# Kernel optimization log

Hardware: AMD Instinct MI355X
Metric: run time of the kernel (lower is better)

The kernel has to match this reference:

```python
import jax, jax.numpy as jnp
import numpy as np

DIM = 1024
N_HEADS = 16
HEAD_DIM = DIM // N_HEADS


def setup_inputs() -> dict:
    key = jax.random.key(0)
    ks = jax.random.split(key, 5)
    B, L = 2, 2048
    q = jax.random.normal(ks[0], (B, L, DIM), dtype=jnp.float32)
    # nn.Linear weights: shape [out_features, in_features], applied as x @ W.T
    scale = 1.0 / np.sqrt(DIM)
    Wq = jax.random.normal(ks[1], (DIM, DIM), dtype=jnp.float32) * scale
    Wk = jax.random.normal(ks[2], (DIM, DIM), dtype=jnp.float32) * scale
    Wv = jax.random.normal(ks[3], (DIM, DIM), dtype=jnp.float32) * scale
    Wo = jax.random.normal(ks[4], (DIM, DIM), dtype=jnp.float32) * scale
    return {"q": q, "Wq": Wq, "Wk": Wk, "Wv": Wv, "Wo": Wo}


def reference(q, Wq, Wk, Wv, Wo):
    B, L, _ = q.shape
    kv = q  # self-attention (kv=None path)
    # projections: x @ W.T, then split heads: b l (h d) -> b h l d
    def split_heads(x):
        return x.reshape(B, L, N_HEADS, HEAD_DIM).transpose(0, 2, 1, 3)
    qh = split_heads(q @ Wq.T)
    kh = split_heads(kv @ Wk.T)
    vh = split_heads(kv @ Wv.T)
    # scaled dot-product attention; scale = sqrt(head_dim)
    scores = jnp.einsum('bhid,bhjd->bhij', qh, kh) / jnp.sqrt(
        jnp.asarray(HEAD_DIM, dtype=qh.dtype))
    attn = jax.nn.softmax(scores, axis=-1)
    out = jnp.einsum('bhij,bhjd->bhid', attn, vh)
    # b h l d -> b l (h d)
    out = out.transpose(0, 2, 1, 3).reshape(B, L, DIM)
    return out @ Wo.T
```

## Files before the change

kernel.cpp:

```cpp
#include <hip/hip_runtime.h>


#define DIMN 1024
#define NH 16
#define HD 64
#define BB 2
#define LL 2048

typedef float f32x4 __attribute__((ext_vector_type(4)));
typedef short s16x8 __attribute__((ext_vector_type(8)));

#define QSCALE 0.18033688011112042f

static __device__ __forceinline__ unsigned short f2bf(float f) {
  unsigned u = __float_as_uint(f);
  u += 0x7fffu + ((u >> 16) & 1u);
  return (unsigned short)(u >> 16);
}
static __device__ __forceinline__ unsigned packbf2(float lo, float hi) {
  return (unsigned)f2bf(lo) | ((unsigned)f2bf(hi) << 16);
}
static __device__ __forceinline__ float xexp2(float x) {
#if __has_builtin(__builtin_amdgcn_exp2f)
  return __builtin_amdgcn_exp2f(x);
#else
  return exp2f(x);
#endif
}
static __device__ __forceinline__ s16x8 cvt8(float4 a, float4 b) {
  s16x8 r;
  r[0] = (short)f2bf(a.x); r[1] = (short)f2bf(a.y);
  r[2] = (short)f2bf(a.z); r[3] = (short)f2bf(a.w);
  r[4] = (short)f2bf(b.x); r[5] = (short)f2bf(b.y);
  r[6] = (short)f2bf(b.z); r[7] = (short)f2bf(b.w);
  return r;
}
static __device__ __forceinline__ void gld16(const unsigned short* g,
                                             unsigned short* l) {
#if __has_builtin(__builtin_amdgcn_global_load_lds)
  __builtin_amdgcn_global_load_lds(
      (const __attribute__((address_space(1))) void*)g,
      (__attribute__((address_space(3))) void*)l, 16, 0, 0);
#else
  ((uint4*)l)[threadIdx.x & 63] = ((const uint4*)g)[0];
#endif
}

static __device__ __forceinline__ int vpos(int s128) {
  return (s128 & 0x60) | ((s128 & 0x0C) << 1) | ((s128 & 0x10) >> 2) | (s128 & 3);
}

__global__ __launch_bounds__(256) void cvt_all(
    const float* __restrict__ X, const float* __restrict__ Wq,
    const float* __restrict__ Wk, const float* __restrict__ Wv,
    const float* __restrict__ Wo, unsigned short* __restrict__ out) {
  const int blk = blockIdx.x;
  const float* src;
  unsigned short* dst;
  size_t off;
  if (blk < 2048) {
    src = X; dst = out; off = (size_t)blk * 2048;
  } else {
    int s = (blk - 2048) >> 9;
    src = (s == 0) ? Wq : (s == 1) ? Wk : (s == 2) ? Wv : Wo;
    dst = out + ((size_t)1 << 22) + (size_t)s * (1u << 20);
    off = (size_t)((blk - 2048) & 511) * 2048;
  }
  size_t i = off + (size_t)threadIdx.x * 8;
  float4 v0 = *(const float4*)(src + i);
  float4 v1 = *(const float4*)(src + i + 4);
  uint4 o;
  o.x = packbf2(v0.x, v0.y); o.y = packbf2(v0.z, v0.w);
  o.z = packbf2(v1.x, v1.y); o.w = packbf2(v1.z, v1.w);
  *(uint4*)(dst + i) = o;
}

__global__ __launch_bounds__(256) void gemm_qkv(
    const unsigned short* __restrict__ Xb, const unsigned short* __restrict__ Wb,
    unsigned short* __restrict__ Qb, unsigned short* __restrict__ Kb,
    unsigned short* __restrict__ VT) {
  __shared__ __align__(16) unsigned short Al[2][128 * 64];
  __shared__ __align__(16) unsigned short Bl[2][128 * 64];
  const int lin = blockIdx.x;
  const int xcd = lin & 7, sblk = lin >> 3;
  const int m0 = ((xcd & 3) * 8 + (sblk & 7)) * 128;
  const int n0g = ((xcd >> 2) * 12 + (sblk >> 3)) * 128;
  const int sel = n0g >> 10;
  const int tid = threadIdx.x;
  const int w = tid >> 6, lane = tid & 63;
  const int c = lane & 15, quad = lane >> 4;
  const int wm = (w & 1) * 64, wn = (w >> 1) * 64;

  f32x4 zero = {0.f, 0.f, 0.f, 0.f};
  f32x4 acc[4][4];
#pragma unroll
  for (int i = 0; i < 4; ++i)
#pragma unroll
    for (int j = 0; j < 4; ++j) acc[i][j] = zero;

  const int l8 = lane >> 3, p8 = lane & 7;
  const unsigned short* gA = Xb + (size_t)(m0 + w * 8 + l8) * DIMN + ((p8 ^ l8) * 8);
  const unsigned short* gB = Wb + (size_t)(n0g + w * 8 + l8) * DIMN + ((p8 ^ l8) * 8);
  const int c7 = c & 7;

#define STAGEQ(buf, k0)                                                       \
  do {                                                                        \
    unsigned short* lA_ = &Al[buf][(w * 8) * 64];                             \
    unsigned short* lB_ = &Bl[buf][(w * 8) * 64];                             \
    _Pragma("unroll")                                                         \
    for (int r = 0; r < 4; ++r) {                                             \
      gld16(gA + (k0) + (size_t)(r * 32) * DIMN, lA_ + r * 32 * 64);          \
      gld16(gB + (k0) + (size_t)(r * 32) * DIMN, lB_ + r * 32 * 64);          \
    }                                                                         \
  } while (0)

  STAGEQ(0, 0);
  __syncthreads();

  for (int t = 0; t < 16; ++t) {
    if (t < 15) STAGEQ((t + 1) & 1, (t + 1) * 64);
    const unsigned short* At = &Al[t & 1][0];
    const unsigned short* Bt = &Bl[t & 1][0];
#pragma unroll
    for (int f = 0; f < 2; ++f) {
      const int rd = ((f * 4 + quad) ^ c7) * 8;
      s16x8 a[4], b[4];
#pragma unroll
      for (int i = 0; i < 4; ++i)
        a[i] = *(const s16x8*)&At[(wm + i * 16 + c) * 64 + rd];
#pragma unroll
      for (int j = 0; j < 4; ++j)
        b[j] = *(const s16x8*)&Bt[(wn + j * 16 + c) * 64 + rd];
      if (sel != 2) {
#pragma unroll
        for (int i = 0; i < 4; ++i)
#pragma unroll
          for (int j = 0; j < 4; ++j)
            acc[i][j] = __builtin_amdgcn_mfma_f32_16x16x32_bf16(b[j], a[i], acc[i][j], 0, 0, 0);
      } else {
#pragma unroll
        for (int i = 0; i < 4; ++i)
#pragma unroll
          for (int j = 0; j < 4; ++j)
            acc[i][j] = __builtin_amdgcn_mfma_f32_16x16x32_bf16(a[i], b[j], acc[i][j], 0, 0, 0);
      }
    }
    __syncthreads();
  }
#undef STAGEQ

  const int n0 = n0g & 1023;
  if (sel != 2) {
    unsigned short* Out = (sel == 0) ? Qb : Kb;
    const float scale = (sel == 0) ? QSCALE : 1.0f;
    const int bi = (m0 + wm) >> 11;
#pragma unroll
    for (int i = 0; i < 4; ++i) {
      const int li = (m0 + wm + i * 16 + c) & 2047;
#pragma unroll
      for (int j = 0; j < 4; ++j) {
        const int nq = n0 + wn + j * 16 + quad * 4;
        const int h = nq >> 6, d = nq & 63;
        uint2 st;
        st.x = packbf2(acc[i][j][0] * scale, acc[i][j][1] * scale);
        st.y = packbf2(acc[i][j][2] * scale, acc[i][j][3] * scale);
        *(uint2*)&Out[(((size_t)bi * NH + h) * LL + li) * HD + d] = st;
      }
    }
  } else {
    const int bi = m0 >> 11;
    const int mlo = m0 & 2047;
#pragma unroll
    for (int i = 0; i < 4; ++i) {
      const int pos = mlo + vpos(wm + i * 16 + quad * 4);
#pragma unroll
      for (int j = 0; j < 4; ++j) {
        const int nv = n0 + wn + j * 16 + c;
        const int h = nv >> 6, d = nv & 63;
        uint2 st;
        st.x = packbf2(acc[i][j][0], acc[i][j][1]);
        st.y = packbf2(acc[i][j][2], acc[i][j][3]);
        *(uint2*)&VT[(((size_t)bi * NH + h) * HD + d) * LL + pos] = st;
      }
    }
  }
}

__global__ __launch_bounds__(256) void gemm_o(
    const unsigned short* __restrict__ A, const unsigned short* __restrict__ Wob,
    float* __restrict__ Out) {
  __shared__ __align__(16) unsigned short Al[2][128 * 64];
  __shared__ __align__(16) unsigned short Bl[2][64 * 64];
  const int lin = blockIdx.x;
  const int xcd = lin & 7, sblk = lin >> 3;
  const int m0 = ((sblk >> 4) * 8 + xcd) * 128;
  const int n0 = (sblk & 15) * 64;
  const int tid = threadIdx.x;
  const int w = tid >> 6, lane = tid & 63;
  const int c = lane & 15, quad = lane >> 4;
  const int wm = (w & 1) * 64, wn = (w >> 1) * 32;

  f32x4 zero = {0.f, 0.f, 0.f, 0.f};
  f32x4 acc[4][2];
#pragma unroll
  for (int i = 0; i < 4; ++i)
#pragma unroll
    for (int j = 0; j < 2; ++j) acc[i][j] = zero;

  const int l8 = lane >> 3, p8 = lane & 7;
  const unsigned short* gA = A + (size_t)(m0 + w * 8 + l8) * DIMN + ((p8 ^ l8) * 8);
  const unsigned short* gB = Wob + (size_t)(n0 + w * 8 + l8) * DIMN + ((p8 ^ l8) * 8);
  const int c7 = c & 7;

#define STAGEO(buf, k0)                                                       \
  do {                                                                        \
    unsigned short* lA_ = &Al[buf][(w * 8) * 64];                             \
    unsigned short* lB_ = &Bl[buf][(w * 8) * 64];                             \
    _Pragma("unroll")                                                         \
    for (int r = 0; r < 4; ++r)                                               \
      gld16(gA + (k0) + (size_t)(r * 32) * DIMN, lA_ + r * 32 * 64);          \
    _Pragma("unroll")                                                         \
    for (int r = 0; r < 2; ++r)                                               \
      gld16(gB + (k0) + (size_t)(r * 32) * DIMN, lB_ + r * 32 * 64);          \
  } while (0)

  STAGEO(0, 0);
  __syncthreads();

  for (int t = 0; t < 16; ++t) {
    if (t < 15) STAGEO((t + 1) & 1, (t + 1) * 64);
    const unsigned short* At = &Al[t & 1][0];
    const unsigned short* Bt = &Bl[t & 1][0];
#pragma unroll
    for (int f = 0; f < 2; ++f) {
      const int rd = ((f * 4 + quad) ^ c7) * 8;
      s16x8 a[4], b[2];
#pragma unroll
      for (int i = 0; i < 4; ++i)
        a[i] = *(const s16x8*)&At[(wm + i * 16 + c) * 64 + rd];
#pragma unroll
      for (int j = 0; j < 2; ++j)
        b[j] = *(const s16x8*)&Bt[(wn + j * 16 + c) * 64 + rd];
#pragma unroll
      for (int i = 0; i < 4; ++i)
#pragma unroll
        for (int j = 0; j < 2; ++j)
          acc[i][j] = __builtin_amdgcn_mfma_f32_16x16x32_bf16(a[i], b[j], acc[i][j], 0, 0, 0);
    }
    __syncthreads();
  }
#undef STAGEO

#pragma unroll
  for (int i = 0; i < 4; ++i)
#pragma unroll
    for (int j = 0; j < 2; ++j)
#pragma unroll
      for (int r = 0; r < 4; ++r)
        Out[(size_t)(m0 + wm + i * 16 + quad * 4 + r) * DIMN + n0 + wn + j * 16 + c] =
            acc[i][j][r];
}

__global__ __launch_bounds__(512, 4) void attn9(
    const unsigned short* __restrict__ Qb, const unsigned short* __restrict__ Kb,
    const unsigned short* __restrict__ VT, unsigned short* __restrict__ AO) {
  __shared__ __align__(16) unsigned short Kl[2][2][64 * 64];
  __shared__ __align__(16) unsigned short Vtl[2][2][64 * 64];

  const int lin = blockIdx.x;
  const int xcd = lin & 7, sblk = lin >> 3;
  const int bh = (sblk >> 4) * 8 + xcd;
  const int qi = sblk & 15;
  const int tid = threadIdx.x;
  const int w = tid >> 6, lane = tid & 63;
  const int half = w >> 2, wl = w & 3;
  const int c = lane & 15, quad = lane >> 4;
  const int qa = qi * 128 + wl * 16;
  const int qbr = qa + 64;

  const unsigned short* Qh = Qb + (size_t)bh * LL * HD;
  const unsigned short* Kh = Kb + (size_t)bh * LL * HD + (size_t)half * 1024 * HD;
  const unsigned short* Vh = VT + (size_t)bh * HD * LL + half * 1024;

  s16x8 qA0 = *(const s16x8*)(Qh + (size_t)(qa + c) * HD + quad * 8);
  s16x8 qA1 = *(const s16x8*)(Qh + (size_t)(qa + c) * HD + 32 + quad * 8);
  s16x8 qB0 = *(const s16x8*)(Qh + (size_t)(qbr + c) * HD + quad * 8);
  s16x8 qB1 = *(const s16x8*)(Qh + (size_t)(qbr + c) * HD + 32 + quad * 8);

  f32x4 zero = {0.f, 0.f, 0.f, 0.f};
  f32x4 oA[4], oB[4];
  float lsumA = 0.f, lsumB = 0.f;
#pragma unroll
  for (int dc = 0; dc < 4; ++dc) { oA[dc] = zero; oB[dc] = zero; }

  const int l8 = lane >> 3, p8 = lane & 7;
  const unsigned short* gK = Kh + (size_t)(wl * 16 + l8) * HD + ((p8 ^ l8) * 8);
  const int vr = wl * 16 + l8;
  const unsigned short* gV = Vh + (size_t)vr * LL + ((p8 ^ l8) * 8);

  const int c7 = c & 7;
  const int kpa = (quad ^ c7) * 8;
  const int kpb = ((quad + 4) ^ c7) * 8;

#define STAGE(buf, kv)                                                        \
  do {                                                                        \
    unsigned short* lK_ = &Kl[half][buf][(wl * 16) * 64];                     \
    unsigned short* lV_ = &Vtl[half][buf][(wl * 16) * 64];                    \
    gld16(gK + (size_t)(kv) * HD, lK_);                                       \
    gld16(gK + (size_t)((kv) + 8) * HD, lK_ + 8 * 64);                        \
    gld16(gV + (kv), lV_);                                                    \
    gld16(gV + (size_t)8 * LL + (kv), lV_ + 8 * 64);                          \
  } while (0)

  STAGE(0, 0);

  for (int it = 0; it < 16; ++it) {
    __syncthreads();
    if (it + 1 < 16) STAGE((it + 1) & 1, (it + 1) * 64);
    const unsigned short* Kt = &Kl[half][it & 1][0];
    const unsigned short* Vt = &Vtl[half][it & 1][0];

    f32x4 sA[4], sB[4];
#pragma unroll
    for (int t4 = 0; t4 < 4; ++t4) {
      const unsigned short* kr = Kt + (t4 * 16 + c) * 64;
      s16x8 kfa = *(const s16x8*)(kr + kpa);
      s16x8 kfb = *(const s16x8*)(kr + kpb);
      sA[t4] = __builtin_amdgcn_mfma_f32_16x16x32_bf16(kfa, qA0, zero, 0, 0, 0);
      sA[t4] = __builtin_amdgcn_mfma_f32_16x16x32_bf16(kfb, qA1, sA[t4], 0, 0, 0);
      sB[t4] = __builtin_amdgcn_mfma_f32_16x16x32_bf16(kfa, qB0, zero, 0, 0, 0);
      sB[t4] = __builtin_amdgcn_mfma_f32_16x16x32_bf16(kfb, qB1, sB[t4], 0, 0, 0);
    }

    float pA[4][4], pB[4][4];
    float a0 = 0.f, a1 = 0.f, b0 = 0.f, b1 = 0.f;
#pragma unroll
    for (int t4 = 0; t4 < 4; ++t4)
#pragma unroll
      for (int r = 0; r < 4; ++r) {
        float eA = xexp2(sA[t4][r]);
        float eB = xexp2(sB[t4][r]);
        pA[t4][r] = eA; pB[t4][r] = eB;
        if (t4 & 1) { a1 += eA; b1 += eB; } else { a0 += eA; b0 += eB; }
      }
    lsumA += a0 + a1; lsumB += b0 + b1;

    s16x8 pfA[2], pfB[2];
#pragma unroll
    for (int kh = 0; kh < 2; ++kh) {
      unsigned puA[4], puB[4];
      puA[0] = __builtin_amdgcn_perm(__float_as_uint(pA[2 * kh][1]),
                                     __float_as_uint(pA[2 * kh][0]), 0x07060302u);
      puA[1] = __builtin_amdgcn_perm(__float_as_uint(pA[2 * kh][3]),
                                     __float_as_uint(pA[2 * kh][2]), 0x07060302u);
      puA[2] = __builtin_amdgcn_perm(__float_as_uint(pA[2 * kh + 1][1]),
                                     __float_as_uint(pA[2 * kh + 1][0]), 0x07060302u);
      puA[3] = __builtin_amdgcn_perm(__float_as_uint(pA[2 * kh + 1][3]),
                                     __float_as_uint(pA[2 * kh + 1][2]), 0x07060302u);
      puB[0] = __builtin_amdgcn_perm(__float_as_uint(pB[2 * kh][1]),
                                     __float_as_uint(pB[2 * kh][0]), 0x07060302u);
      puB[1] = __builtin_amdgcn_perm(__float_as_uint(pB[2 * kh][3]),
                                     __float_as_uint(pB[2 * kh][2]), 0x07060302u);
      puB[2] = __builtin_amdgcn_perm(__float_as_uint(pB[2 * kh + 1][1]),
                                     __float_as_uint(pB[2 * kh + 1][0]), 0x07060302u);
      puB[3] = __builtin_amdgcn_perm(__float_as_uint(pB[2 * kh + 1][3]),
                                     __float_as_uint(pB[2 * kh + 1][2]), 0x07060302u);
      pfA[kh] = *(const s16x8*)puA;
      pfB[kh] = *(const s16x8*)puB;
    }

#pragma unroll
    for (int kh = 0; kh < 2; ++kh) {
#pragma unroll
      for (int dc = 0; dc < 4; ++dc) {
        s16x8 vf = *(const s16x8*)(Vt + (dc * 16 + c) * 64 +
                                   (((kh * 4 + quad) ^ c7) * 8));
        oA[dc] = __builtin_amdgcn_mfma_f32_16x16x32_bf16(vf, pfA[kh], oA[dc], 0, 0, 0);
        oB[dc] = __builtin_amdgcn_mfma_f32_16x16x32_bf16(vf, pfB[kh], oB[dc], 0, 0, 0);
      }
    }
  }
#undef STAGE

  float lA = lsumA;
  lA += __shfl_xor(lA, 16);
  lA += __shfl_xor(lA, 32);
  float lB = lsumB;
  lB += __shfl_xor(lB, 16);
  lB += __shfl_xor(lB, 32);

  f32x4* ob4 = (f32x4*)&Kl[0][0][0];
  float* lb = (float*)&Vtl[0][0][0];

  __syncthreads();
  if (half == 1) {
#pragma unroll
    for (int dc = 0; dc < 4; ++dc) {
      ob4[((wl * 2 + 0) * 4 + dc) * 64 + lane] = oA[dc];
      ob4[((wl * 2 + 1) * 4 + dc) * 64 + lane] = oB[dc];
    }
    lb[(wl * 2 + 0) * 64 + lane] = lA;
    lb[(wl * 2 + 1) * 64 + lane] = lB;
  }
  __syncthreads();
  if (half == 0) {
    lA += lb[(wl * 2 + 0) * 64 + lane];
    lB += lb[(wl * 2 + 1) * 64 + lane];
    float invA = 1.0f / lA;
    float invB = 1.0f / lB;
    const int bi = bh >> 4, h = bh & 15;
    unsigned short* dstA = AO + ((size_t)bi * LL + qa + c) * DIMN + h * HD + quad * 4;
    unsigned short* dstB = AO + ((size_t)bi * LL + qbr + c) * DIMN + h * HD + quad * 4;
#pragma unroll
    for (int dc = 0; dc < 4; ++dc) {
      f32x4 sa = oA[dc] + ob4[((wl * 2 + 0) * 4 + dc) * 64 + lane];
      f32x4 sb = oB[dc] + ob4[((wl * 2 + 1) * 4 + dc) * 64 + lane];
      uint2 stA, stB;
      stA.x = packbf2(sa[0] * invA, sa[1] * invA);
      stA.y = packbf2(sa[2] * invA, sa[3] * invA);
      stB.x = packbf2(sb[0] * invB, sb[1] * invB);
      stB.y = packbf2(sb[2] * invB, sb[3] * invB);
      *(uint2*)(dstA + dc * 16) = stA;
      *(uint2*)(dstB + dc * 16) = stB;
    }
  }
}

__global__ __launch_bounds__(64) void qkv_proj_f(
    const float* __restrict__ X, const float* __restrict__ Wq,
    const float* __restrict__ Wk, const float* __restrict__ Wv,
    unsigned short* __restrict__ Qb, unsigned short* __restrict__ Kb,
    unsigned short* __restrict__ VT) {
  const int m0 = blockIdx.x * 64;
  const int n0g = blockIdx.y * 64;
  const int sel = n0g >> 10;
  const int n0 = n0g & 1023;
  const float* W = (sel == 0) ? Wq : (sel == 1) ? Wk : Wv;
  const int lane = threadIdx.x;
  const int c = lane & 15, quad = lane >> 4;

  f32x4 zero = {0.f, 0.f, 0.f, 0.f};
  f32x4 acc[4][4];
#pragma unroll
  for (int i = 0; i < 4; ++i)
#pragma unroll
    for (int j = 0; j < 4; ++j) acc[i][j] = zero;

  const float* ab = X + (size_t)(m0 + c) * DIMN + quad * 8;
  const float* bb = W + (size_t)(n0 + c) * DIMN + quad * 8;

  for (int k0 = 0; k0 < DIMN; k0 += 32) {
    s16x8 a[4], b[4];
#pragma unroll
    for (int i = 0; i < 4; ++i) {
      const float* pp = ab + i * 16 * DIMN + k0;
      a[i] = cvt8(*(const float4*)pp, *(const float4*)(pp + 4));
    }
#pragma unroll
    for (int j = 0; j < 4; ++j) {
      const float* pp = bb + j * 16 * DIMN + k0;
      b[j] = cvt8(*(const float4*)pp, *(const float4*)(pp + 4));
    }
    if (sel != 2) {
#pragma unroll
      for (int i = 0; i < 4; ++i)
#pragma unroll
        for (int j = 0; j < 4; ++j)
          acc[i][j] = __builtin_amdgcn_mfma_f32_16x16x32_bf16(a[i], b[j], acc[i][j], 0, 0, 0);
    } else {
#pragma unroll
      for (int i = 0; i < 4; ++i)
#pragma unroll
        for (int j = 0; j < 4; ++j)
          acc[i][j] = __builtin_amdgcn_mfma_f32_16x16x32_bf16(b[j], a[i], acc[i][j], 0, 0, 0);
    }
  }

  if (sel != 2) {
    unsigned short* Out = (sel == 0) ? Qb : Kb;
    const float scale = (sel == 0) ? QSCALE : 1.0f;
#pragma unroll
    for (int i = 0; i < 4; ++i)
#pragma unroll
      for (int j = 0; j < 4; ++j)
#pragma unroll
        for (int r = 0; r < 4; ++r) {
          int row = m0 + i * 16 + quad * 4 + r;
          int nl = n0 + j * 16 + c;
          int bi = row >> 11, li = row & 2047;
          int h = nl >> 6, d = nl & 63;
          Out[(((size_t)bi * NH + h) * LL + li) * HD + d] = f2bf(acc[i][j][r] * scale);
        }
  } else {
#pragma unroll
    for (int i = 0; i < 4; ++i) {
#pragma unroll
      for (int j = 0; j < 4; ++j)
#pragma unroll
        for (int r = 0; r < 4; ++r) {
          int n = n0 + j * 16 + quad * 4 + r;
          int s128 = (m0 & 64) + i * 16 + c;
          int m = (m0 & ~127) + vpos(s128);
          int h = n >> 6, d = n & 63;
          int bi = m0 >> 11;
          VT[(((size_t)bi * NH + h) * HD + d) * LL + (m & 2047)] = f2bf(acc[i][j][r]);
        }
    }
  }
}

__global__ __launch_bounds__(64) void o_proj_f(
    const unsigned short* __restrict__ A, const float* __restrict__ Wo,
    float* __restrict__ Out) {
  const int m0 = blockIdx.x * 64, n0 = blockIdx.y * 64;
  const int lane = threadIdx.x;
  const int c = lane & 15, quad = lane >> 4;

  f32x4 zero = {0.f, 0.f, 0.f, 0.f};
  f32x4 acc[4][4];
#pragma unroll
  for (int i = 0; i < 4; ++i)
#pragma unroll
    for (int j = 0; j < 4; ++j) acc[i][j] = zero;

  const unsigned short* ab = A + (size_t)(m0 + c) * DIMN + quad * 8;
  const float* bb = Wo + (size_t)(n0 + c) * DIMN + quad * 8;

  for (int k0 = 0; k0 < DIMN; k0 += 32) {
    s16x8 a[4], b[4];
#pragma unroll
    for (int i = 0; i < 4; ++i) a[i] = *(const s16x8*)(ab + i * 16 * DIMN + k0);
#pragma unroll
    for (int j = 0; j < 4; ++j) {
      const float* pp = bb + j * 16 * DIMN + k0;
      b[j] = cvt8(*(const float4*)pp, *(const float4*)(pp + 4));
    }
#pragma unroll
    for (int i = 0; i < 4; ++i)
#pragma unroll
      for (int j = 0; j < 4; ++j)
        acc[i][j] = __builtin_amdgcn_mfma_f32_16x16x32_bf16(a[i], b[j], acc[i][j], 0, 0, 0);
  }

#pragma unroll
  for (int i = 0; i < 4; ++i)
#pragma unroll
    for (int j = 0; j < 4; ++j)
#pragma unroll
      for (int r = 0; r < 4; ++r)
        Out[(size_t)(m0 + i * 16 + quad * 4 + r) * DIMN + n0 + j * 16 + c] = acc[i][j][r];
}

extern "C" void kernel_launch(void* const* d_in, const int* in_sizes, int n_in,
                              void* d_out, int out_size, void* d_ws, size_t ws_size,
                              hipStream_t stream) {
  const float* X = (const float*)d_in[0];
  const float* Wq = (const float*)d_in[1];
  const float* Wk = (const float*)d_in[2];
  const float* Wv = (const float*)d_in[3];
  const float* Wo = (const float*)d_in[4];
  float* Out = (float*)d_out;

  const size_t M1 = (size_t)1 << 20;
  unsigned short* ws16 = (unsigned short*)d_ws;

  if (ws_size >= (size_t)48 * 1024 * 1024) {
    unsigned short* Xb = ws16;
    unsigned short* Wb = ws16 + 4 * M1;
    unsigned short* Qb = ws16 + 8 * M1;
    unsigned short* Kb = ws16 + 12 * M1;
    unsigned short* VT = ws16 + 16 * M1;
    unsigned short* AO = ws16 + 20 * M1;
    cvt_all<<<4096, 256, 0, stream>>>(X, Wq, Wk, Wv, Wo, ws16);
    gemm_qkv<<<768, 256, 0, stream>>>(Xb, Wb, Qb, Kb, VT);
    attn9<<<512, 512, 0, stream>>>(Qb, Kb, VT, AO);
    gemm_o<<<512, 256, 0, stream>>>(AO, Wb + 3 * M1, Out);
  } else {
    unsigned short* Qb = ws16;
    unsigned short* Kb = ws16 + 4 * M1;
    unsigned short* VT = ws16 + 8 * M1;
    unsigned short* AO = ws16 + 12 * M1;
    qkv_proj_f<<<dim3(64, 48), 64, 0, stream>>>(X, Wq, Wk, Wv, Qb, Kb, VT);
    attn9<<<512, 512, 0, stream>>>(Qb, Kb, VT, AO);
    o_proj_f<<<dim3(64, 16), 64, 0, stream>>>(AO, Wo, Out);
  }
}
```

Measured before the change: 178.2 us.

## Single-buffer QKV GEMM LDS and widen O-projection tiles with vector stores

The QKV projection GEMM drops its double-buffered LDS staging for a single buffer with a sync before and after each load, which halves LDS use and may allow more resident blocks but no longer overlaps loads with MFMA work. The output projection GEMM moves from 128x64 to 128x128 tiles (256 blocks instead of 512), swaps the MFMA operand order, and writes results as 16-byte float4 vectors instead of scalar stores. The larger tiles cut redundant A-tile reads and store instructions, at the cost of fewer blocks on the device and more accumulator registers.

```diff
diff --git a/kernel.cpp b/kernel.cpp
--- a/kernel.cpp
+++ b/kernel.cpp
@@ -79,8 +79,8 @@
     const unsigned short* __restrict__ Xb, const unsigned short* __restrict__ Wb,
     unsigned short* __restrict__ Qb, unsigned short* __restrict__ Kb,
     unsigned short* __restrict__ VT) {
-  __shared__ __align__(16) unsigned short Al[2][128 * 64];
-  __shared__ __align__(16) unsigned short Bl[2][128 * 64];
+  __shared__ __align__(16) unsigned short Al[128 * 64];
+  __shared__ __align__(16) unsigned short Bl[128 * 64];
   const int lin = blockIdx.x;
   const int xcd = lin & 7, sblk = lin >> 3;
   const int m0 = ((xcd & 3) * 8 + (sblk & 7)) * 128;
@@ -101,9 +101,108 @@
   const int l8 = lane >> 3, p8 = lane & 7;
   const unsigned short* gA = Xb + (size_t)(m0 + w * 8 + l8) * DIMN + ((p8 ^ l8) * 8);
   const unsigned short* gB = Wb + (size_t)(n0g + w * 8 + l8) * DIMN + ((p8 ^ l8) * 8);
+  unsigned short* lA = Al + (w * 8) * 64;
+  unsigned short* lB = Bl + (w * 8) * 64;
   const int c7 = c & 7;
 
-#define STAGEQ(buf, k0)                                                       \
+  for (int k0 = 0; k0 < DIMN; k0 += 64) {
+    __syncthreads();
+#pragma unroll
+    for (int r = 0; r < 4; ++r) {
+      gld16(gA + k0 + (size_t)(r * 32) * DIMN, lA + r * 32 * 64);
+      gld16(gB + k0 + (size_t)(r * 32) * DIMN, lB + r * 32 * 64);
+    }
+    __syncthreads();
+#pragma unroll
+    for (int f = 0; f < 2; ++f) {
+      const int rd = ((f * 4 + quad) ^ c7) * 8;
+      s16x8 a[4], b[4];
+#pragma unroll
+      for (int i = 0; i < 4; ++i)
+        a[i] = *(const s16x8*)&Al[(wm + i * 16 + c) * 64 + rd];
+#pragma unroll
+      for (int j = 0; j < 4; ++j)
+        b[j] = *(const s16x8*)&Bl[(wn + j * 16 + c) * 64 + rd];
+      if (sel != 2) {
+#pragma unroll
+        for (int i = 0; i < 4; ++i)
+#pragma unroll
+          for (int j = 0; j < 4; ++j)
+            acc[i][j] = __builtin_amdgcn_mfma_f32_16x16x32_bf16(b[j], a[i], acc[i][j], 0, 0, 0);
+      } else {
+#pragma unroll
+        for (int i = 0; i < 4; ++i)
+#pragma unroll
+          for (int j = 0; j < 4; ++j)
+            acc[i][j] = __builtin_amdgcn_mfma_f32_16x16x32_bf16(a[i], b[j], acc[i][j], 0, 0, 0);
+      }
+    }
+  }
+
+  const int n0 = n0g & 1023;
+  if (sel != 2) {
+    unsigned short* Out = (sel == 0) ? Qb : Kb;
+    const float scale = (sel == 0) ? QSCALE : 1.0f;
+    const int bi = (m0 + wm) >> 11;
+#pragma unroll
+    for (int i = 0; i < 4; ++i) {
+      const int li = (m0 + wm + i * 16 + c) & 2047;
+#pragma unroll
+      for (int j = 0; j < 4; ++j) {
+        const int nq = n0 + wn + j * 16 + quad * 4;
+        const int h = nq >> 6, d = nq & 63;
+        uint2 st;
+        st.x = packbf2(acc[i][j][0] * scale, acc[i][j][1] * scale);
+        st.y = packbf2(acc[i][j][2] * scale, acc[i][j][3] * scale);
+        *(uint2*)&Out[(((size_t)bi * NH + h) * LL + li) * HD + d] = st;
+      }
+    }
+  } else {
+    const int bi = m0 >> 11;
+    const int mlo = m0 & 2047;
+#pragma unroll
+    for (int i = 0; i < 4; ++i) {
+      const int pos = mlo + vpos(wm + i * 16 + quad * 4);
+#pragma unroll
+      for (int j = 0; j < 4; ++j) {
+        const int nv = n0 + wn + j * 16 + c;
+        const int h = nv >> 6, d = nv & 63;
+        uint2 st;
+        st.x = packbf2(acc[i][j][0], acc[i][j][1]);
+        st.y = packbf2(acc[i][j][2], acc[i][j][3]);
+        *(uint2*)&VT[(((size_t)bi * NH + h) * HD + d) * LL + pos] = st;
+      }
+    }
+  }
+}
+
+__global__ __launch_bounds__(256) void gemm_o(
+    const unsigned short* __restrict__ A, const unsigned short* __restrict__ Wob,
+    float* __restrict__ Out) {
+  __shared__ __align__(16) unsigned short Al[2][128 * 64];
+  __shared__ __align__(16) unsigned short Bl[2][128 * 64];
+  const int lin = blockIdx.x;
+  const int xcd = lin & 7, sblk = lin >> 3;
+  const int m0 = (xcd * 4 + (sblk >> 3)) * 128;
+  const int n0 = (sblk & 7) * 128;
+  const int tid = threadIdx.x;
+  const int w = tid >> 6, lane = tid & 63;
+  const int c = lane & 15, quad = lane >> 4;
+  const int wm = (w & 1) * 64, wn = (w >> 1) * 64;
+
+  f32x4 zero = {0.f, 0.f, 0.f, 0.f};
+  f32x4 acc[4][4];
+#pragma unroll
+  for (int i = 0; i < 4; ++i)
+#pragma unroll
+    for (int j = 0; j < 4; ++j) acc[i][j] = zero;
+
+  const int l8 = lane >> 3, p8 = lane & 7;
+  const unsigned short* gA = A + (size_t)(m0 + w * 8 + l8) * DIMN + ((p8 ^ l8) * 8);
+  const unsigned short* gB = Wob + (size_t)(n0 + w * 8 + l8) * DIMN + ((p8 ^ l8) * 8);
+  const int c7 = c & 7;
+
+#define STAGEO(buf, k0)                                                       \
   do {                                                                        \
     unsigned short* lA_ = &Al[buf][(w * 8) * 64];                             \
     unsigned short* lB_ = &Bl[buf][(w * 8) * 64];                             \
@@ -114,116 +213,6 @@
     }                                                                         \
   } while (0)
 
-  STAGEQ(0, 0);
-  __syncthreads();
-
-  for (int t = 0; t < 16; ++t) {
-    if (t < 15) STAGEQ((t + 1) & 1, (t + 1) * 64);
-    const unsigned short* At = &Al[t & 1][0];
-    const unsigned short* Bt = &Bl[t & 1][0];
-#pragma unroll
-    for (int f = 0; f < 2; ++f) {
-      const int rd = ((f * 4 + quad) ^ c7) * 8;
-      s16x8 a[4], b[4];
-#pragma unroll
-      for (int i = 0; i < 4; ++i)
-        a[i] = *(const s16x8*)&At[(wm + i * 16 + c) * 64 + rd];
-#pragma unroll
-      for (int j = 0; j < 4; ++j)
-        b[j] = *(const s16x8*)&Bt[(wn + j * 16 + c) * 64 + rd];
-      if (sel != 2) {
-#pragma unroll
-        for (int i = 0; i < 4; ++i)
-#pragma unroll
-          for (int j = 0; j < 4; ++j)
-            acc[i][j] = __builtin_amdgcn_mfma_f32_16x16x32_bf16(b[j], a[i], acc[i][j], 0, 0, 0);
-      } else {
-#pragma unroll
-        for (int i = 0; i < 4; ++i)
-#pragma unroll
-          for (int j = 0; j < 4; ++j)
-            acc[i][j] = __builtin_amdgcn_mfma_f32_16x16x32_bf16(a[i], b[j], acc[i][j], 0, 0, 0);
-      }
-    }
-    __syncthreads();
-  }
-#undef STAGEQ
-
-  const int n0 = n0g & 1023;
-  if (sel != 2) {
-    unsigned short* Out = (sel == 0) ? Qb : Kb;
-    const float scale = (sel == 0) ? QSCALE : 1.0f;
-    const int bi = (m0 + wm) >> 11;
-#pragma unroll
-    for (int i = 0; i < 4; ++i) {
-      const int li = (m0 + wm + i * 16 + c) & 2047;
-#pragma unroll
-      for (int j = 0; j < 4; ++j) {
-        const int nq = n0 + wn + j * 16 + quad * 4;
-        const int h = nq >> 6, d = nq & 63;
-        uint2 st;
-        st.x = packbf2(acc[i][j][0] * scale, acc[i][j][1] * scale);
-        st.y = packbf2(acc[i][j][2] * scale, acc[i][j][3] * scale);
-        *(uint2*)&Out[(((size_t)bi * NH + h) * LL + li) * HD + d] = st;
-      }
-    }
-  } else {
-    const int bi = m0 >> 11;
-    const int mlo = m0 & 2047;
-#pragma unroll
-    for (int i = 0; i < 4; ++i) {
-      const int pos = mlo + vpos(wm + i * 16 + quad * 4);
-#pragma unroll
-      for (int j = 0; j < 4; ++j) {
-        const int nv = n0 + wn + j * 16 + c;
-        const int h = nv >> 6, d = nv & 63;
-        uint2 st;
-        st.x = packbf2(acc[i][j][0], acc[i][j][1]);
-        st.y = packbf2(acc[i][j][2], acc[i][j][3]);
-        *(uint2*)&VT[(((size_t)bi * NH + h) * HD + d) * LL + pos] = st;
-      }
-    }
-  }
-}
-
-__global__ __launch_bounds__(256) void gemm_o(
-    const unsigned short* __restrict__ A, const unsigned short* __restrict__ Wob,
-    float* __restrict__ Out) {
-  __shared__ __align__(16) unsigned short Al[2][128 * 64];
-  __shared__ __align__(16) unsigned short Bl[2][64 * 64];
-  const int lin = blockIdx.x;
-  const int xcd = lin & 7, sblk = lin >> 3;
-  const int m0 = ((sblk >> 4) * 8 + xcd) * 128;
-  const int n0 = (sblk & 15) * 64;
-  const int tid = threadIdx.x;
-  const int w = tid >> 6, lane = tid & 63;
-  const int c = lane & 15, quad = lane >> 4;
-  const int wm = (w & 1) * 64, wn = (w >> 1) * 32;
-
-  f32x4 zero = {0.f, 0.f, 0.f, 0.f};
-  f32x4 acc[4][2];
-#pragma unroll
-  for (int i = 0; i < 4; ++i)
-#pragma unroll
-    for (int j = 0; j < 2; ++j) acc[i][j] = zero;
-
-  const int l8 = lane >> 3, p8 = lane & 7;
-  const unsigned short* gA = A + (size_t)(m0 + w * 8 + l8) * DIMN + ((p8 ^ l8) * 8);
-  const unsigned short* gB = Wob + (size_t)(n0 + w * 8 + l8) * DIMN + ((p8 ^ l8) * 8);
-  const int c7 = c & 7;
-
-#define STAGEO(buf, k0)                                                       \
-  do {                                                                        \
-    unsigned short* lA_ = &Al[buf][(w * 8) * 64];                             \
-    unsigned short* lB_ = &Bl[buf][(w * 8) * 64];                             \
-    _Pragma("unroll")                                                         \
-    for (int r = 0; r < 4; ++r)                                               \
-      gld16(gA + (k0) + (size_t)(r * 32) * DIMN, lA_ + r * 32 * 64);          \
-    _Pragma("unroll")                                                         \
-    for (int r = 0; r < 2; ++r)                                               \
-      gld16(gB + (k0) + (size_t)(r * 32) * DIMN, lB_ + r * 32 * 64);          \
-  } while (0)
-
   STAGEO(0, 0);
   __syncthreads();
 
@@ -234,31 +223,32 @@
 #pragma unroll
     for (int f = 0; f < 2; ++f) {
       const int rd = ((f * 4 + quad) ^ c7) * 8;
-      s16x8 a[4], b[2];
+      s16x8 a[4], b[4];
 #pragma unroll
       for (int i = 0; i < 4; ++i)
         a[i] = *(const s16x8*)&At[(wm + i * 16 + c) * 64 + rd];
 #pragma unroll
-      for (int j = 0; j < 2; ++j)
+      for (int j = 0; j < 4; ++j)
         b[j] = *(const s16x8*)&Bt[(wn + j * 16 + c) * 64 + rd];
 #pragma unroll
       for (int i = 0; i < 4; ++i)
 #pragma unroll
-        for (int j = 0; j < 2; ++j)
-          acc[i][j] = __builtin_amdgcn_mfma_f32_16x16x32_bf16(a[i], b[j], acc[i][j], 0, 0, 0);
+        for (int j = 0; j < 4; ++j)
+          acc[i][j] = __builtin_amdgcn_mfma_f32_16x16x32_bf16(b[j], a[i], acc[i][j], 0, 0, 0);
     }
     __syncthreads();
   }
 #undef STAGEO
 
 #pragma unroll
-  for (int i = 0; i < 4; ++i)
-#pragma unroll
-    for (int j = 0; j < 2; ++j)
-#pragma unroll
-      for (int r = 0; r < 4; ++r)
-        Out[(size_t)(m0 + wm + i * 16 + quad * 4 + r) * DIMN + n0 + wn + j * 16 + c] =
-            acc[i][j][r];
+  for (int i = 0; i < 4; ++i) {
+    const int mi = m0 + wm + i * 16 + c;
+#pragma unroll
+    for (int j = 0; j < 4; ++j) {
+      const int nq = n0 + wn + j * 16 + quad * 4;
+      *(f32x4*)&Out[(size_t)mi * DIMN + nq] = acc[i][j];
+    }
+  }
 }
 
 __global__ __launch_bounds__(512, 4) void attn9(
@@ -574,7 +564,7 @@
     cvt_all<<<4096, 256, 0, stream>>>(X, Wq, Wk, Wv, Wo, ws16);
     gemm_qkv<<<768, 256, 0, stream>>>(Xb, Wb, Qb, Kb, VT);
     attn9<<<512, 512, 0, stream>>>(Qb, Kb, VT, AO);
-    gemm_o<<<512, 256, 0, stream>>>(AO, Wb + 3 * M1, Out);
+    gemm_o<<<256, 256, 0, stream>>>(AO, Wb + 3 * M1, Out);
   } else {
     unsigned short* Qb = ws16;
     unsigned short* Kb = ws16 + 4 * M1;
```

Result: slower. 182.1 us (+2.2%).

## Halve GEMM K-tile to 32 with new swizzled LDS layout; add MFMA setprio in attention

Applied to the files above, without the earlier changes.

Both projection GEMMs now stage K-slices of 32 instead of 64 per iteration. The LDS tiles are repacked so two rows share one 64-element line with an XOR swizzle, which halves shared memory per block and doubles the loop trip count. The aim is to raise occupancy and cut LDS footprint, at the cost of twice as many barriers per K. The attention kernel also wraps its MFMA sections in s_setprio so waves in the matrix phase get issue priority over waves doing softmax.

```diff
diff --git a/kernel.cpp b/kernel.cpp
--- a/kernel.cpp
+++ b/kernel.cpp
@@ -79,8 +79,8 @@
     const unsigned short* __restrict__ Xb, const unsigned short* __restrict__ Wb,
     unsigned short* __restrict__ Qb, unsigned short* __restrict__ Kb,
     unsigned short* __restrict__ VT) {
-  __shared__ __align__(16) unsigned short Al[2][128 * 64];
-  __shared__ __align__(16) unsigned short Bl[2][128 * 64];
+  __shared__ __align__(16) unsigned short Al[2][64 * 64];
+  __shared__ __align__(16) unsigned short Bl[2][64 * 64];
   const int lin = blockIdx.x;
   const int xcd = lin & 7, sblk = lin >> 3;
   const int m0 = ((xcd & 3) * 8 + (sblk & 7)) * 128;
@@ -99,51 +99,56 @@
     for (int j = 0; j < 4; ++j) acc[i][j] = zero;
 
   const int l8 = lane >> 3, p8 = lane & 7;
-  const unsigned short* gA = Xb + (size_t)(m0 + w * 8 + l8) * DIMN + ((p8 ^ l8) * 8);
-  const unsigned short* gB = Wb + (size_t)(n0g + w * 8 + l8) * DIMN + ((p8 ^ l8) * 8);
-  const int c7 = c & 7;
+  const int lc = p8 ^ l8, halfc = lc >> 2, qc = (lc & 3) * 8;
+  const unsigned short* gA0 =
+      Xb + (size_t)(m0 + w * 32 + l8 * 2 + halfc) * DIMN + qc;
+  const unsigned short* gA1 =
+      Xb + (size_t)(m0 + w * 32 + 16 + l8 * 2 + halfc) * DIMN + qc;
+  const unsigned short* gB0 =
+      Wb + (size_t)(n0g + w * 32 + l8 * 2 + halfc) * DIMN + qc;
+  const unsigned short* gB1 =
+      Wb + (size_t)(n0g + w * 32 + 16 + l8 * 2 + halfc) * DIMN + qc;
+
+  const int pc = (((c & 1) << 2) | quad) ^ (c >> 1);
+  const int aoff = ((wm >> 1) + (c >> 1)) * 64 + pc * 8;
+  const int boff = ((wn >> 1) + (c >> 1)) * 64 + pc * 8;
 
 #define STAGEQ(buf, k0)                                                       \
   do {                                                                        \
-    unsigned short* lA_ = &Al[buf][(w * 8) * 64];                             \
-    unsigned short* lB_ = &Bl[buf][(w * 8) * 64];                             \
-    _Pragma("unroll")                                                         \
-    for (int r = 0; r < 4; ++r) {                                             \
-      gld16(gA + (k0) + (size_t)(r * 32) * DIMN, lA_ + r * 32 * 64);          \
-      gld16(gB + (k0) + (size_t)(r * 32) * DIMN, lB_ + r * 32 * 64);          \
-    }                                                                         \
+    unsigned short* lA_ = &Al[buf][(w * 16) * 64];                            \
+    unsigned short* lB_ = &Bl[buf][(w * 16) * 64];                            \
+    gld16(gA0 + (k0), lA_);                                                   \
+    gld16(gA1 + (k0), lA_ + 8 * 64);                                          \
+    gld16(gB0 + (k0), lB_);                                                   \
+    gld16(gB1 + (k0), lB_ + 8 * 64);                                          \
   } while (0)
 
   STAGEQ(0, 0);
   __syncthreads();
 
-  for (int t = 0; t < 16; ++t) {
-    if (t < 15) STAGEQ((t + 1) & 1, (t + 1) * 64);
+  for (int t = 0; t < 32; ++t) {
+    if (t < 31) STAGEQ((t + 1) & 1, (t + 1) * 32);
     const unsigned short* At = &Al[t & 1][0];
     const unsigned short* Bt = &Bl[t & 1][0];
-#pragma unroll
-    for (int f = 0; f < 2; ++f) {
-      const int rd = ((f * 4 + quad) ^ c7) * 8;
-      s16x8 a[4], b[4];
+    s16x8 a[4], b[4];
+#pragma unroll
+    for (int i = 0; i < 4; ++i)
+      a[i] = *(const s16x8*)&At[aoff + i * 8 * 64];
+#pragma unroll
+    for (int j = 0; j < 4; ++j)
+      b[j] = *(const s16x8*)&Bt[boff + j * 8 * 64];
+    if (sel != 2) {
 #pragma unroll
       for (int i = 0; i < 4; ++i)
-        a[i] = *(const s16x8*)&At[(wm + i * 16 + c) * 64 + rd];
-#pragma unroll
-      for (int j = 0; j < 4; ++j)
-        b[j] = *(const s16x8*)&Bt[(wn + j * 16 + c) * 64 + rd];
-      if (sel != 2) {
-#pragma unroll
-        for (int i = 0; i < 4; ++i)
-#pragma unroll
-          for (int j = 0; j < 4; ++j)
-            acc[i][j] = __builtin_amdgcn_mfma_f32_16x16x32_bf16(b[j], a[i], acc[i][j], 0, 0, 0);
-      } else {
-#pragma unroll
-        for (int i = 0; i < 4; ++i)
-#pragma unroll
-          for (int j = 0; j < 4; ++j)
-            acc[i][j] = __builtin_amdgcn_mfma_f32_16x16x32_bf16(a[i], b[j], acc[i][j], 0, 0, 0);
-      }
+#pragma unroll
+        for (int j = 0; j < 4; ++j)
+          acc[i][j] = __builtin_amdgcn_mfma_f32_16x16x32_bf16(b[j], a[i], acc[i][j], 0, 0, 0);
+    } else {
+#pragma unroll
+      for (int i = 0; i < 4; ++i)
+#pragma unroll
+        for (int j = 0; j < 4; ++j)
+          acc[i][j] = __builtin_amdgcn_mfma_f32_16x16x32_bf16(a[i], b[j], acc[i][j], 0, 0, 0);
     }
     __syncthreads();
   }
@@ -189,8 +194,8 @@
 __global__ __launch_bounds__(256) void gemm_o(
     const unsigned short* __restrict__ A, const unsigned short* __restrict__ Wob,
     float* __restrict__ Out) {
-  __shared__ __align__(16) unsigned short Al[2][128 * 64];
-  __shared__ __align__(16) unsigned short Bl[2][64 * 64];
+  __shared__ __align__(16) unsigned short Al[2][64 * 64];
+  __shared__ __align__(16) unsigned short Bl[2][32 * 64];
   const int lin = blockIdx.x;
   const int xcd = lin & 7, sblk = lin >> 3;
   const int m0 = ((sblk >> 4) * 8 + xcd) * 128;
@@ -208,45 +213,46 @@
     for (int j = 0; j < 2; ++j) acc[i][j] = zero;
 
   const int l8 = lane >> 3, p8 = lane & 7;
-  const unsigned short* gA = A + (size_t)(m0 + w * 8 + l8) * DIMN + ((p8 ^ l8) * 8);
-  const unsigned short* gB = Wob + (size_t)(n0 + w * 8 + l8) * DIMN + ((p8 ^ l8) * 8);
-  const int c7 = c & 7;
+  const int lc = p8 ^ l8, halfc = lc >> 2, qc = (lc & 3) * 8;
+  const unsigned short* gA0 =
+      A + (size_t)(m0 + w * 32 + l8 * 2 + halfc) * DIMN + qc;
+  const unsigned short* gA1 =
+      A + (size_t)(m0 + w * 32 + 16 + l8 * 2 + halfc) * DIMN + qc;
+  const unsigned short* gB0 =
+      Wob + (size_t)(n0 + w * 16 + l8 * 2 + halfc) * DIMN + qc;
+
+  const int pc = (((c & 1) << 2) | quad) ^ (c >> 1);
+  const int aoff = ((wm >> 1) + (c >> 1)) * 64 + pc * 8;
+  const int boff = ((wn >> 1) + (c >> 1)) * 64 + pc * 8;
 
 #define STAGEO(buf, k0)                                                       \
   do {                                                                        \
-    unsigned short* lA_ = &Al[buf][(w * 8) * 64];                             \
+    unsigned short* lA_ = &Al[buf][(w * 16) * 64];                            \
     unsigned short* lB_ = &Bl[buf][(w * 8) * 64];                             \
-    _Pragma("unroll")                                                         \
-    for (int r = 0; r < 4; ++r)                                               \
-      gld16(gA + (k0) + (size_t)(r * 32) * DIMN, lA_ + r * 32 * 64);          \
-    _Pragma("unroll")                                                         \
-    for (int r = 0; r < 2; ++r)                                               \
-      gld16(gB + (k0) + (size_t)(r * 32) * DIMN, lB_ + r * 32 * 64);          \
+    gld16(gA0 + (k0), lA_);                                                   \
+    gld16(gA1 + (k0), lA_ + 8 * 64);                                          \
+    gld16(gB0 + (k0), lB_);                                                   \
   } while (0)
 
   STAGEO(0, 0);
   __syncthreads();
 
-  for (int t = 0; t < 16; ++t) {
-    if (t < 15) STAGEO((t + 1) & 1, (t + 1) * 64);
+  for (int t = 0; t < 32; ++t) {
+    if (t < 31) STAGEO((t + 1) & 1, (t + 1) * 32);
     const unsigned short* At = &Al[t & 1][0];
     const unsigned short* Bt = &Bl[t & 1][0];
-#pragma unroll
-    for (int f = 0; f < 2; ++f) {
-      const int rd = ((f * 4 + quad) ^ c7) * 8;
-      s16x8 a[4], b[2];
-#pragma unroll
-      for (int i = 0; i < 4; ++i)
-        a[i] = *(const s16x8*)&At[(wm + i * 16 + c) * 64 + rd];
+    s16x8 a[4], b[2];
+#pragma unroll
+    for (int i = 0; i < 4; ++i)
+      a[i] = *(const s16x8*)&At[aoff + i * 8 * 64];
+#pragma unroll
+    for (int j = 0; j < 2; ++j)
+      b[j] = *(const s16x8*)&Bt[boff + j * 8 * 64];
+#pragma unroll
+    for (int i = 0; i < 4; ++i)
 #pragma unroll
       for (int j = 0; j < 2; ++j)
-        b[j] = *(const s16x8*)&Bt[(wn + j * 16 + c) * 64 + rd];
-#pragma unroll
-      for (int i = 0; i < 4; ++i)
-#pragma unroll
-        for (int j = 0; j < 2; ++j)
-          acc[i][j] = __builtin_amdgcn_mfma_f32_16x16x32_bf16(a[i], b[j], acc[i][j], 0, 0, 0);
-    }
+        acc[i][j] = __builtin_amdgcn_mfma_f32_16x16x32_bf16(a[i], b[j], acc[i][j], 0, 0, 0);
     __syncthreads();
   }
 #undef STAGEO
@@ -321,6 +327,7 @@
     const unsigned short* Vt = &Vtl[half][it & 1][0];
 
     f32x4 sA[4], sB[4];
+    __builtin_amdgcn_s_setprio(1);
 #pragma unroll
     for (int t4 = 0; t4 < 4; ++t4) {
       const unsigned short* kr = Kt + (t4 * 16 + c) * 64;
@@ -331,6 +338,7 @@
       sB[t4] = __builtin_amdgcn_mfma_f32_16x16x32_bf16(kfa, qB0, zero, 0, 0, 0);
       sB[t4] = __builtin_amdgcn_mfma_f32_16x16x32_bf16(kfb, qB1, sB[t4], 0, 0, 0);
     }
+    __builtin_amdgcn_s_setprio(0);
 
     float pA[4][4], pB[4][4];
     float a0 = 0.f, a1 = 0.f, b0 = 0.f, b1 = 0.f;
@@ -369,6 +377,7 @@
       pfB[kh] = *(const s16x8*)puB;
     }
 
+    __builtin_amdgcn_s_setprio(1);
 #pragma unroll
     for (int kh = 0; kh < 2; ++kh) {
 #pragma unroll
@@ -379,6 +388,7 @@
         oB[dc] = __builtin_amdgcn_mfma_f32_16x16x32_bf16(vf, pfB[kh], oB[dc], 0, 0, 0);
       }
     }
+    __builtin_amdgcn_s_setprio(0);
   }
 #undef STAGE
 
```

Result: slower. 195.6 us (+9.8%).
